# Performance work log

Hardware: AMD Instinct MI355X
Metric: run time of the kernel (lower is better)

The kernel has to match this reference:

```python
import jax, jax.numpy as jnp
import numpy as np

N = 50000      # nodes
E = 800000     # edges (avg degree 16)
F_IN = 256
F_OUT = 256


def setup_inputs() -> dict:
    key = jax.random.key(0)
    ks = jax.random.split(key, 8)
    feature = jax.random.normal(ks[0], (N, F_IN), dtype=jnp.float32)
    e_w = jax.random.uniform(ks[1], (E, 1), dtype=jnp.float32)
    snorm_n = jnp.ones((N, 1), dtype=jnp.float32)
    snorm_e = jnp.ones((E, 1), dtype=jnp.float32)
    src = jax.random.randint(ks[2], (E,), 0, N, dtype=jnp.int32)
    dst = jax.random.randint(ks[3], (E,), 0, N, dtype=jnp.int32)
    scale = 1.0 / np.sqrt(F_IN)
    W_self = jax.random.normal(ks[4], (F_IN, F_OUT), dtype=jnp.float32) * scale
    W = jax.random.normal(ks[5], (F_IN, F_OUT), dtype=jnp.float32) * scale
    b = jax.random.normal(ks[6], (F_OUT,), dtype=jnp.float32) * scale
    return {"feature": feature, "e_w": e_w, "snorm_n": snorm_n,
            "snorm_e": snorm_e, "W_self": W_self, "W": W, "b": b,
            "src": src, "dst": dst}


def reference(feature, e_w, snorm_n, snorm_e, W_self, W, b, src, dst):
    n = feature.shape[0]
    ones_e = jnp.ones_like(src, dtype=feature.dtype)
    # self transform
    h_s = feature @ W_self                                   # [N, F_OUT]
    # source-side degree normalization: deg_out^{-1/2}
    out_deg = jnp.maximum(jax.ops.segment_sum(ones_e, src, num_segments=n), 1.0)
    feat = feature * (out_deg ** -0.5)[:, None]              # [N, F_IN]
    # message = h[src] * e_w, aggregated by sum into dst (u_mul_e + sum reduce)
    msgs = feat[src] * e_w                                   # [E, F_IN]
    agg = jax.ops.segment_sum(msgs, dst, num_segments=n)     # [N, F_IN]
    # neighbor transform + destination-side degree normalization
    h = agg @ W + b                                          # [N, F_OUT]
    in_deg = jnp.maximum(jax.ops.segment_sum(ones_e, dst, num_segments=n), 1.0)
    h = h * (in_deg ** -0.5)[:, None]
    return h_s + h, e_w
```

## Files before the change

### kernel.cpp

```cpp
#include <hip/hip_runtime.h>
#include <hip/hip_bf16.h>

#define N_NODES 50000
#define N_EDGES 800000

#define ROW_TILES    391
#define WCONV_BLOCKS 512
#define EDGE_BLOCKS  782
#define K1_BLOCKS    2346
#define SCAN_BLOCKS  196

typedef __bf16 bf16x8_t __attribute__((ext_vector_type(8)));
typedef float  f32x4_t  __attribute__((ext_vector_type(4)));

__device__ __forceinline__ unsigned short f2bf(float x) {
  __hip_bfloat16 h = __float2bfloat16(x);
  return __builtin_bit_cast(unsigned short, h);
}
__device__ __forceinline__ float bf2f(unsigned short u) {
  unsigned int v = ((unsigned int)u) << 16;
  return __builtin_bit_cast(float, v);
}
__device__ __forceinline__ unsigned int pk2(float lo, float hi) {
  return ((unsigned int)f2bf(hi) << 16) | (unsigned int)f2bf(lo);
}

__global__ __launch_bounds__(256) void wconv_kernel(
    const float* __restrict__ Wself, const float* __restrict__ W,
    unsigned short* __restrict__ Bt)
{
  int idx = blockIdx.x * 256 + threadIdx.x;
  int n = idx >> 8, k = idx & 255;
  float v = (n < 256) ? Wself[k * 256 + n] : W[k * 256 + (n - 256)];
  Bt[idx] = f2bf(v);
}

__global__ __launch_bounds__(256, 4) void gemm_edge_kernel(
    const float* __restrict__ feature,
    const unsigned short* __restrict__ Bt,
    const float* __restrict__ e_w, const int* __restrict__ src, const int* __restrict__ dst,
    int* __restrict__ cnt_in, int* __restrict__ cnt_out,
    unsigned char* __restrict__ rank8, float* __restrict__ out1,
    float* __restrict__ out0,
    unsigned char* __restrict__ y8)
{
  const int b   = blockIdx.x;
  const int tid = threadIdx.x;

  if (b % 3 == 2) {
    const int e0 = (b / 3) * 1024 + tid;
#pragma unroll
    for (int k = 0; k < 4; ++k) {
      int e = e0 + k * 256;
      if (e < N_EDGES) {
        int s = src[e], d = dst[e];
        out1[e] = e_w[e];
        atomicAdd(&cnt_out[s], 1);
        rank8[e] = (unsigned char)atomicAdd(&cnt_in[d], 1);
      }
    }
    return;
  }

  __shared__ __align__(16) unsigned short As[2][128 * 32];
  __shared__ __align__(16) unsigned short Bs[2][128 * 32];

  const int g    = (b / 3) * 2 + (b % 3);
  const int q    = g & 3;
  const int m0   = (g >> 2) * 128;
  const int bn0  = q * 128;
  const int lane = tid & 63;
  const int wave = tid >> 6;
  const int wm   = (wave & 1) * 64;
  const int wn   = (wave >> 1) * 64;
  const int fr   = lane & 15;
  const int fkc  = lane >> 4;

  const int ra = tid >> 1, ha = tid & 1;
  const int sA = (ra >> 1) & 3;
  const int arow = (m0 + ra < N_NODES) ? (m0 + ra) : 0;
  const float* aptr = feature + (size_t)arow * 256 + ha * 16;
  const int aw0 = ra * 32 + (((2 * ha) ^ sA) * 8);
  const int aw1 = ra * 32 + ((((2 * ha) | 1) ^ sA) * 8);

  f32x4_t acc[4][4] = {};

  {
#pragma unroll
    for (int i = 0; i < 2; ++i) {
      int r  = i * 64 + (tid >> 2);
      int cg = (tid & 3) ^ ((r >> 1) & 3);
      const unsigned short* gb = Bt + (size_t)(bn0 + r) * 256 + cg * 8;
      __builtin_amdgcn_global_load_lds((const __attribute__((address_space(1))) void*)gb,
                                       (__attribute__((address_space(3))) void*)&Bs[0][i * 2048 + wave * 512],
                                       16, 0, 0);
    }
    float4 a0 = *(const float4*)(aptr + 0);
    float4 a1 = *(const float4*)(aptr + 4);
    float4 a2 = *(const float4*)(aptr + 8);
    float4 a3 = *(const float4*)(aptr + 12);
    uint4 p0, p1;
    p0.x = pk2(a0.x, a0.y); p0.y = pk2(a0.z, a0.w);
    p0.z = pk2(a1.x, a1.y); p0.w = pk2(a1.z, a1.w);
    p1.x = pk2(a2.x, a2.y); p1.y = pk2(a2.z, a2.w);
    p1.z = pk2(a3.x, a3.y); p1.w = pk2(a3.z, a3.w);
    *(uint4*)&As[0][aw0] = p0;
    *(uint4*)&As[0][aw1] = p1;
  }
  __syncthreads();

#pragma unroll
  for (int s = 0; s < 8; ++s) {
    const int cb = s & 1, nb = cb ^ 1;
    float4 a0, a1, a2, a3;
    if (s < 7) {
      const int k0 = (s + 1) * 32;
#pragma unroll
      for (int i = 0; i < 2; ++i) {
        int r  = i * 64 + (tid >> 2);
        int cg = (tid & 3) ^ ((r >> 1) & 3);
        const unsigned short* gb = Bt + (size_t)(bn0 + r) * 256 + k0 + cg * 8;
        __builtin_amdgcn_global_load_lds((const __attribute__((address_space(1))) void*)gb,
                                         (__attribute__((address_space(3))) void*)&Bs[nb][i * 2048 + wave * 512],
                                         16, 0, 0);
      }
      a0 = *(const float4*)(aptr + k0 + 0);
      a1 = *(const float4*)(aptr + k0 + 4);
      a2 = *(const float4*)(aptr + k0 + 8);
      a3 = *(const float4*)(aptr + k0 + 12);
    }

    bf16x8_t af[4], bv[4];
#pragma unroll
    for (int i = 0; i < 4; ++i) {
      int R = wm + i * 16 + fr;
      af[i] = *(const bf16x8_t*)&As[cb][R * 32 + ((fkc ^ ((R >> 1) & 3)) * 8)];
    }
#pragma unroll
    for (int j = 0; j < 4; ++j) {
      int R = wn + j * 16 + fr;
      bv[j] = *(const bf16x8_t*)&Bs[cb][R * 32 + ((fkc ^ ((R >> 1) & 3)) * 8)];
    }
#pragma unroll
    for (int i = 0; i < 4; ++i)
#pragma unroll
      for (int j = 0; j < 4; ++j)
        acc[i][j] = __builtin_amdgcn_mfma_f32_16x16x32_bf16(af[i], bv[j], acc[i][j], 0, 0, 0);

    if (s < 7) {
      uint4 p0, p1;
      p0.x = pk2(a0.x, a0.y); p0.y = pk2(a0.z, a0.w);
      p0.z = pk2(a1.x, a1.y); p0.w = pk2(a1.z, a1.w);
      p1.x = pk2(a2.x, a2.y); p1.y = pk2(a2.z, a2.w);
      p1.z = pk2(a3.x, a3.y); p1.w = pk2(a3.z, a3.w);
      *(uint4*)&As[nb][aw0] = p0;
      *(uint4*)&As[nb][aw1] = p1;
      __syncthreads();
    }
  }

  if (q < 2) {
    const int cbase = q * 128 + wn + (lane & 15);
#pragma unroll
    for (int i = 0; i < 4; ++i) {
      int rowb = m0 + wm + i * 16 + (lane >> 4) * 4;
#pragma unroll
      for (int j = 0; j < 4; ++j) {
        int col = cbase + j * 16;
#pragma unroll
        for (int r = 0; r < 4; ++r) {
          int row = rowb + r;
          if (row < N_NODES)
            out0[(size_t)row * 256 + col] = acc[i][j][r];
        }
      }
    }
  } else {
    const int cbase = (q - 2) * 128 + wn + (lane & 15);
#pragma unroll
    for (int i = 0; i < 4; ++i) {
      int rowb = m0 + wm + i * 16 + (lane >> 4) * 4;
#pragma unroll
      for (int j = 0; j < 4; ++j) {
        int col = cbase + j * 16;
#pragma unroll
        for (int r = 0; r < 4; ++r) {
          int row = rowb + r;
          if (row < N_NODES) {
            float ys = acc[i][j][r];
            unsigned int pk = (unsigned int)__builtin_amdgcn_cvt_pk_fp8_f32(ys, ys, 0, false);
            y8[(size_t)row * 256 + col] = (unsigned char)(pk & 0xffu);
          }
        }
      }
    }
  }
}

__global__ __launch_bounds__(256) void scan1_kernel(
    const int* __restrict__ cnt, int* __restrict__ sums)
{
  int idx = blockIdx.x * 256 + threadIdx.x;
  int v = (idx < N_NODES) ? cnt[idx] : 0;
#pragma unroll
  for (int d = 32; d; d >>= 1) v += __shfl_down(v, d);
  __shared__ int sm[4];
  if ((threadIdx.x & 63) == 0) sm[threadIdx.x >> 6] = v;
  __syncthreads();
  if (threadIdx.x == 0) sums[blockIdx.x] = sm[0] + sm[1] + sm[2] + sm[3];
}

__global__ __launch_bounds__(256) void scan2_kernel(int* __restrict__ sums)
{
  const int t = threadIdx.x;
  int v = (t < SCAN_BLOCKS) ? sums[t] : 0;
  __shared__ int sm[256];
  sm[t] = v;
  __syncthreads();
  for (int d = 1; d < 256; d <<= 1) {
    int u = (t >= d) ? sm[t - d] : 0;
    __syncthreads();
    sm[t] += u;
    __syncthreads();
  }
  if (t < SCAN_BLOCKS) sums[t] = sm[t] - v;
}

__global__ __launch_bounds__(256) void scan3_kernel(
    const int* __restrict__ cnt, const int* __restrict__ sums, int* __restrict__ off)
{
  const int t = threadIdx.x;
  int idx = blockIdx.x * 256 + t;
  int v = (idx < N_NODES) ? cnt[idx] : 0;
  __shared__ int sm[256];
  sm[t] = v;
  __syncthreads();
  for (int d = 1; d < 256; d <<= 1) {
    int u = (t >= d) ? sm[t - d] : 0;
    __syncthreads();
    sm[t] += u;
    __syncthreads();
  }
  if (idx <= N_NODES) off[idx] = sm[t] - v + sums[blockIdx.x];
}

__global__ __launch_bounds__(256) void scatter_kernel(
    const float* __restrict__ e_w, const int* __restrict__ src, const int* __restrict__ dst,
    const unsigned char* __restrict__ rank8, const int* __restrict__ off,
    unsigned int* __restrict__ csr)
{
  const int e0 = blockIdx.x * 1024 + threadIdx.x;
#pragma unroll
  for (int k = 0; k < 4; ++k) {
    int e = e0 + k * 256;
    if (e < N_EDGES) {
      int d = dst[e];
      int r = rank8[e];
      float w = e_w[e];
      int s = src[e];
      csr[off[d] + r] = ((unsigned int)f2bf(w) << 16) | (unsigned int)s;
    }
  }
}

__global__ __launch_bounds__(256) void agg_kernel(
    const unsigned char* __restrict__ y8, const unsigned int* __restrict__ csr,
    const int* __restrict__ off, const int* __restrict__ cnt_out,
    const float* __restrict__ bias, float* __restrict__ out0)
{
  const int hw   = threadIdx.x >> 5;
  const int lane = threadIdx.x & 31;
  const int node = blockIdx.x * 8 + hw;
  if (node >= N_NODES) return;
  const int base = off[node];
  const int deg  = off[node + 1] - base;

  float a0 = 0.f, a1 = 0.f, a2 = 0.f, a3 = 0.f;
  float a4 = 0.f, a5 = 0.f, a6 = 0.f, a7 = 0.f;

  for (int bb = 0; bb < deg; bb += 32) {
    int idx = bb + lane;
    unsigned int ent = (idx < deg) ? csr[base + idx] : 0u;
    int   sl = (int)(ent & 0xffffu);
    float wl = bf2f((unsigned short)(ent >> 16));
    int co = cnt_out[sl]; if (co < 1) co = 1;
    wl *= rsqrtf((float)co);

#pragma unroll
    for (int t0 = 0; t0 < 32; t0 += 16) {
      if (bb + t0 >= deg) break;
#pragma unroll
      for (int t = 0; t < 16; ++t) {
        int eb = t0 + t;
        int   s = __shfl(sl, eb, 32);
        float w = __shfl(wl, eb, 32);
        uint2 u = *(const uint2*)(y8 + (size_t)s * 256 + lane * 8);
        a0 += w * __builtin_amdgcn_cvt_f32_fp8(u.x, 0);
        a1 += w * __builtin_amdgcn_cvt_f32_fp8(u.x, 1);
        a2 += w * __builtin_amdgcn_cvt_f32_fp8(u.x, 2);
        a3 += w * __builtin_amdgcn_cvt_f32_fp8(u.x, 3);
        a4 += w * __builtin_amdgcn_cvt_f32_fp8(u.y, 0);
        a5 += w * __builtin_amdgcn_cvt_f32_fp8(u.y, 1);
        a6 += w * __builtin_amdgcn_cvt_f32_fp8(u.y, 2);
        a7 += w * __builtin_amdgcn_cvt_f32_fp8(u.y, 3);
      }
    }
  }

  int dn = deg < 1 ? 1 : deg;
  float inv = rsqrtf((float)dn);
  float4 b0 = *(const float4*)(bias + lane * 8);
  float4 b1 = *(const float4*)(bias + lane * 8 + 4);
  size_t offo = (size_t)node * 256 + lane * 8;
  float4 o0 = *(float4*)(out0 + offo);
  float4 o1 = *(float4*)(out0 + offo + 4);
  o0.x += (a0 + b0.x) * inv;  o0.y += (a1 + b0.y) * inv;
  o0.z += (a2 + b0.z) * inv;  o0.w += (a3 + b0.w) * inv;
  o1.x += (a4 + b1.x) * inv;  o1.y += (a5 + b1.y) * inv;
  o1.z += (a6 + b1.z) * inv;  o1.w += (a7 + b1.w) * inv;
  *(float4*)(out0 + offo)     = o0;
  *(float4*)(out0 + offo + 4) = o1;
}

extern "C" void kernel_launch(void* const* d_in, const int* in_sizes, int n_in,
                              void* d_out, int out_size, void* d_ws, size_t ws_size,
                              hipStream_t stream) {
  const float* feature = (const float*)d_in[0];
  const float* e_w     = (const float*)d_in[1];
  const float* W_self  = (const float*)d_in[4];
  const float* W       = (const float*)d_in[5];
  const float* bias    = (const float*)d_in[6];
  const int*   src     = (const int*)d_in[7];
  const int*   dst     = (const int*)d_in[8];

  float* out0 = (float*)d_out;
  float* out1 = out0 + (size_t)N_NODES * 256;

  char* ws = (char*)d_ws;
  int*            cnt_in  = (int*)(ws + 0);
  int*            cnt_out = (int*)(ws + 262144);
  int*            off     = (int*)(ws + 524288);
  unsigned char*  rank8   = (unsigned char*)(ws + 786432);
  int*            sums    = (int*)(ws + 1638400);
  unsigned int*   csr     = (unsigned int*)(ws + 1835008);
  unsigned short* Bt      = (unsigned short*)(ws + 5242880);
  unsigned char*  y8      = (unsigned char*)(ws + 5767168);

  hipMemsetAsync(ws, 0, 524288, stream);

  wconv_kernel<<<WCONV_BLOCKS, 256, 0, stream>>>(W_self, W, Bt);
  gemm_edge_kernel<<<K1_BLOCKS, 256, 0, stream>>>(
      feature, Bt, e_w, src, dst, cnt_in, cnt_out, rank8, out1, out0, y8);
  scan1_kernel<<<SCAN_BLOCKS, 256, 0, stream>>>(cnt_in, sums);
  scan2_kernel<<<1, 256, 0, stream>>>(sums);
  scan3_kernel<<<SCAN_BLOCKS, 256, 0, stream>>>(cnt_in, sums, off);
  scatter_kernel<<<EDGE_BLOCKS, 256, 0, stream>>>(e_w, src, dst, rank8, off, csr);
  agg_kernel<<<(N_NODES + 7) / 8, 256, 0, stream>>>(y8, csr, off, cnt_out, bias, out0);
}
```

Measured before the change: 263.1 us.

## Store self-transform in bf16 scratch and reorder histogram/GEMM block schedule

The self-transform GEMM output is now written as bf16 into a workspace buffer instead of fp32 into the output, and the aggregation kernel reads it and writes the final output once rather than doing a read-modify-write of fp32. This halves intermediate traffic for h_s and removes one full fp32 output read. The block schedule also changes so all histogram blocks come first, and GEMM tiles are remapped with a swizzle across column quarters, which may change L2 reuse of A rows. Storing h_s in bf16 adds rounding error to the result.

```diff
diff --git a/kernel.cpp b/kernel.cpp
--- a/kernel.cpp
+++ b/kernel.cpp
@@ -5,13 +5,16 @@
 #define N_EDGES 800000
 
 #define ROW_TILES    391
+#define HIST_BLOCKS  782
+#define GEMM_SPACE   1568
+#define K1_BLOCKS    (HIST_BLOCKS + GEMM_SPACE)
 #define WCONV_BLOCKS 512
+#define SCAN_BLOCKS  196
 #define EDGE_BLOCKS  782
-#define K1_BLOCKS    2346
-#define SCAN_BLOCKS  196
 
 typedef __bf16 bf16x8_t __attribute__((ext_vector_type(8)));
 typedef float  f32x4_t  __attribute__((ext_vector_type(4)));
+typedef unsigned short u16x8 __attribute__((ext_vector_type(8)));
 
 __device__ __forceinline__ unsigned short f2bf(float x) {
   __hip_bfloat16 h = __float2bfloat16(x);
@@ -41,14 +44,14 @@
     const float* __restrict__ e_w, const int* __restrict__ src, const int* __restrict__ dst,
     int* __restrict__ cnt_in, int* __restrict__ cnt_out,
     unsigned char* __restrict__ rank8, float* __restrict__ out1,
-    float* __restrict__ out0,
+    unsigned short* __restrict__ hs16,
     unsigned char* __restrict__ y8)
 {
   const int b   = blockIdx.x;
   const int tid = threadIdx.x;
 
-  if (b % 3 == 2) {
-    const int e0 = (b / 3) * 1024 + tid;
+  if (b < HIST_BLOCKS) {
+    const int e0 = b * 1024 + tid;
 #pragma unroll
     for (int k = 0; k < 4; ++k) {
       int e = e0 + k * 256;
@@ -62,12 +65,15 @@
     return;
   }
 
+  const int u  = b - HIST_BLOCKS;
+  const int q  = (u >> 3) & 3;
+  const int t  = (u >> 5) * 8 + (((u & 7) + 6) & 7);
+  if (t >= ROW_TILES) return;
+
   __shared__ __align__(16) unsigned short As[2][128 * 32];
   __shared__ __align__(16) unsigned short Bs[2][128 * 32];
 
-  const int g    = (b / 3) * 2 + (b % 3);
-  const int q    = g & 3;
-  const int m0   = (g >> 2) * 128;
+  const int m0   = t * 128;
   const int bn0  = q * 128;
   const int lane = tid & 63;
   const int wave = tid >> 6;
@@ -171,7 +177,7 @@
         for (int r = 0; r < 4; ++r) {
           int row = rowb + r;
           if (row < N_NODES)
-            out0[(size_t)row * 256 + col] = acc[i][j][r];
+            hs16[(size_t)row * 256 + col] = f2bf(acc[i][j][r]);
         }
       }
     }
@@ -266,6 +272,7 @@
 __global__ __launch_bounds__(256) void agg_kernel(
     const unsigned char* __restrict__ y8, const unsigned int* __restrict__ csr,
     const int* __restrict__ off, const int* __restrict__ cnt_out,
+    const unsigned short* __restrict__ hs16,
     const float* __restrict__ bias, float* __restrict__ out0)
 {
   const int hw   = threadIdx.x >> 5;
@@ -309,15 +316,19 @@
 
   int dn = deg < 1 ? 1 : deg;
   float inv = rsqrtf((float)dn);
+  size_t offo = (size_t)node * 256 + lane * 8;
+  u16x8 hv = *(const u16x8*)(hs16 + offo);
   float4 b0 = *(const float4*)(bias + lane * 8);
   float4 b1 = *(const float4*)(bias + lane * 8 + 4);
-  size_t offo = (size_t)node * 256 + lane * 8;
-  float4 o0 = *(float4*)(out0 + offo);
-  float4 o1 = *(float4*)(out0 + offo + 4);
-  o0.x += (a0 + b0.x) * inv;  o0.y += (a1 + b0.y) * inv;
-  o0.z += (a2 + b0.z) * inv;  o0.w += (a3 + b0.w) * inv;
-  o1.x += (a4 + b1.x) * inv;  o1.y += (a5 + b1.y) * inv;
-  o1.z += (a6 + b1.z) * inv;  o1.w += (a7 + b1.w) * inv;
+  float4 o0, o1;
+  o0.x = bf2f(hv[0]) + (a0 + b0.x) * inv;
+  o0.y = bf2f(hv[1]) + (a1 + b0.y) * inv;
+  o0.z = bf2f(hv[2]) + (a2 + b0.z) * inv;
+  o0.w = bf2f(hv[3]) + (a3 + b0.w) * inv;
+  o1.x = bf2f(hv[4]) + (a4 + b1.x) * inv;
+  o1.y = bf2f(hv[5]) + (a5 + b1.y) * inv;
+  o1.z = bf2f(hv[6]) + (a6 + b1.z) * inv;
+  o1.w = bf2f(hv[7]) + (a7 + b1.w) * inv;
   *(float4*)(out0 + offo)     = o0;
   *(float4*)(out0 + offo + 4) = o1;
 }
@@ -345,15 +356,16 @@
   unsigned int*   csr     = (unsigned int*)(ws + 1835008);
   unsigned short* Bt      = (unsigned short*)(ws + 5242880);
   unsigned char*  y8      = (unsigned char*)(ws + 5767168);
+  unsigned short* hs16    = (unsigned short*)(ws + 18567168);
 
   hipMemsetAsync(ws, 0, 524288, stream);
 
   wconv_kernel<<<WCONV_BLOCKS, 256, 0, stream>>>(W_self, W, Bt);
   gemm_edge_kernel<<<K1_BLOCKS, 256, 0, stream>>>(
-      feature, Bt, e_w, src, dst, cnt_in, cnt_out, rank8, out1, out0, y8);
+      feature, Bt, e_w, src, dst, cnt_in, cnt_out, rank8, out1, hs16, y8);
   scan1_kernel<<<SCAN_BLOCKS, 256, 0, stream>>>(cnt_in, sums);
   scan2_kernel<<<1, 256, 0, stream>>>(sums);
   scan3_kernel<<<SCAN_BLOCKS, 256, 0, stream>>>(cnt_in, sums, off);
   scatter_kernel<<<EDGE_BLOCKS, 256, 0, stream>>>(e_w, src, dst, rank8, off, csr);
-  agg_kernel<<<(N_NODES + 7) / 8, 256, 0, stream>>>(y8, csr, off, cnt_out, bias, out0);
-}
+  agg_kernel<<<(N_NODES + 7) / 8, 256, 0, stream>>>(y8, csr, off, cnt_out, hs16, bias, out0);
+}
```

After: 283.5 us. +7.7%, slower.
